# Kernel optimization log

Measured on AMD Instinct MI355X. Metric: run time of the kernel, lower is better.

## Reference

```python
import jax, jax.numpy as jnp
import numpy as np

SLOPE = 0.15  # LeakyReLU negative slope used throughout the module

def leaky(v):
    return jnp.where(v >= 0, v, SLOPE * v)

def _linear_params(key, fan_in, fan_out):
    kw, kb = jax.random.split(key)
    bound = 1.0 / np.sqrt(fan_in)
    W = jax.random.uniform(kw, (fan_in, fan_out), minval=-bound, maxval=bound, dtype=jnp.float32)
    b = jax.random.uniform(kb, (fan_out,), minval=-bound, maxval=bound, dtype=jnp.float32)
    return W, b

N_NODES = 50000
N_EDGES = 640000
IN_DIM = 128
EDGE_DIM = 64
HID = 128
LAT = 64

def setup_inputs() -> dict:
    key = jax.random.key(0)
    ks = jax.random.split(key, 12)
    x = jax.random.normal(ks[0], (N_NODES, IN_DIM), dtype=jnp.float32)
    edge_index = jax.random.randint(ks[1], (2, N_EDGES), 0, N_NODES, dtype=jnp.int32)
    edge_attr = jax.random.normal(ks[2], (N_EDGES, EDGE_DIM), dtype=jnp.float32)
    # conv1 params
    e1W1, e1b1 = _linear_params(ks[3], EDGE_DIM, HID)
    e1W2, e1b2 = _linear_params(ks[4], HID, HID)
    n1W, n1b = _linear_params(ks[5], IN_DIM + HID, HID)
    # conv2 params
    e2W1, e2b1 = _linear_params(ks[6], EDGE_DIM, HID)
    e2W2, e2b2 = _linear_params(ks[7], HID, HID)
    n2W, n2b = _linear_params(ks[8], HID + HID, HID)
    muW, mub = _linear_params(ks[9], HID, LAT)
    lvW, lvb = _linear_params(ks[10], HID, LAT)
    return {"x": x, "edge_index": edge_index, "edge_attr": edge_attr,
            "e1W1": e1W1, "e1b1": e1b1, "e1W2": e1W2, "e1b2": e1b2, "n1W": n1W, "n1b": n1b,
            "e2W1": e2W1, "e2b1": e2b1, "e2W2": e2W2, "e2b2": e2b2, "n2W": n2W, "n2b": n2b,
            "muW": muW, "mub": mub, "lvW": lvW, "lvb": lvb}

def edge_encoder(x, edge_index, edge_attr, eW1, eb1, eW2, eb2, nW, nb):
    # edge MLP: Linear -> LeakyReLU(0.15) -> Linear
    emb = leaky(edge_attr @ eW1 + eb1) @ eW2 + eb2           # [E, H]
    dst = edge_index[1]                                       # PyG x_i = x[target]
    z = jnp.concatenate([x[dst], emb], axis=1)                # [E, in+H]
    msg = z @ nW + nb                                         # [E, H]
    return jax.ops.segment_sum(msg, dst, num_segments=x.shape[0])  # aggr='add'

def reference(x, edge_index, edge_attr,
              e1W1, e1b1, e1W2, e1b2, n1W, n1b,
              e2W1, e2b1, e2W2, e2b2, n2W, n2b,
              muW, mub, lvW, lvb):
    # Dropout is identity in eval mode.
    h = leaky(edge_encoder(x, edge_index, edge_attr, e1W1, e1b1, e1W2, e1b2, n1W, n1b))
    h = leaky(edge_encoder(h, edge_index, edge_attr, e2W1, e2b1, e2W2, e2b2, n2W, n2b))
    mu = h @ muW + mub
    logvar = h @ lvW + lvb
    return (mu, logvar)
```

## Files before the change

kernel.cpp:

```cpp
#include <hip/hip_runtime.h>

typedef __bf16 bf16x4 __attribute__((ext_vector_type(4)));
typedef __bf16 bf16x8 __attribute__((ext_vector_type(8)));
typedef float  f32x4  __attribute__((ext_vector_type(4)));

constexpr int N_NODES = 50000;
constexpr int N_EDGES = 640000;
constexpr int NTILES  = 98;
constexpr int NB_EDGE = 2500;

__device__ __forceinline__ float leaky(float v) { return v >= 0.f ? v : 0.15f * v; }

__global__ void prep_kernel(
    const float* __restrict__ e1W1, const float* __restrict__ e1b1,
    const float* __restrict__ e1W2, const float* __restrict__ e1b2,
    const float* __restrict__ n1W,  const float* __restrict__ n1b,
    const float* __restrict__ e2W1, const float* __restrict__ e2b1,
    const float* __restrict__ e2W2, const float* __restrict__ e2b2,
    const float* __restrict__ n2W,  const float* __restrict__ n2b,
    const float* __restrict__ muW,  const float* __restrict__ mub,
    const float* __restrict__ lvW,  const float* __restrict__ lvb,
    __bf16* __restrict__ packE, __bf16* __restrict__ packN1,
    __bf16* __restrict__ packN2, __bf16* __restrict__ packH,
    float* __restrict__ ebias, float* __restrict__ c1, float* __restrict__ c2,
    float* __restrict__ hbias)
{
    int bid = blockIdx.x;
    int lane = threadIdx.x;
    int quad = lane >> 4, low = lane & 15;

    if (bid < 32) {
        int ct = bid >> 1, kt = bid & 1;
        for (int j = 0; j < 8; ++j) {
            int k = kt * 32 + quad * 8 + j;
            int n = ct * 16 + low;
            float v = (n < 128) ? e1W1[k * 128 + n] : e2W1[k * 128 + (n - 128)];
            packE[((ct * 2 + kt) * 64 + lane) * 8 + j] = (__bf16)v;
        }
    } else if (bid < 160) {
        bool is1 = bid < 96;
        int tile = bid - (is1 ? 32 : 96);
        const float* nW  = is1 ? n1W  : n2W;
        const float* eW2 = is1 ? e1W2 : e2W2;
        __bf16* dst = is1 ? packN1 : packN2;
        int ct = tile >> 3, kt = tile & 7;
        for (int j = 0; j < 8; ++j) {
            int k = kt * 32 + quad * 8 + j;
            int n = ct * 16 + low;
            float v;
            if (k < 128) {
                v = nW[k * 128 + n];
            } else {
                int i = k - 128;
                float acc = 0.f;
                for (int k2 = 0; k2 < 128; ++k2)
                    acc += eW2[i * 128 + k2] * nW[(128 + k2) * 128 + n];
                v = acc;
            }
            dst[((ct * 8 + kt) * 64 + lane) * 8 + j] = (__bf16)v;
        }
    } else if (bid < 192) {
        int tile = bid - 160;
        int ct = tile >> 2, kt = tile & 3;
        for (int j = 0; j < 8; ++j) {
            int k = kt * 32 + quad * 8 + j;
            int n = ct * 16 + low;
            float v = (n < 64) ? muW[k * 64 + n] : lvW[k * 64 + (n - 64)];
            packH[((ct * 4 + kt) * 64 + lane) * 8 + j] = (__bf16)v;
        }
    } else if (bid == 192 || bid == 193) {
        const float* nW  = (bid == 192) ? n1W  : n2W;
        const float* nb  = (bid == 192) ? n1b  : n2b;
        const float* eb2 = (bid == 192) ? e1b2 : e2b2;
        float* dst = (bid == 192) ? c1 : c2;
        for (int rep = 0; rep < 2; ++rep) {
            int j = lane + rep * 64;
            float acc = nb[j];
            for (int k = 0; k < 128; ++k)
                acc += eb2[k] * nW[(128 + k) * 128 + j];
            dst[j] = acc;
        }
    } else {
        for (int rep = 0; rep < 4; ++rep) {
            int j = lane + rep * 64;
            ebias[j] = (j < 128) ? e1b1[j] : e2b1[j - 128];
        }
        for (int rep = 0; rep < 2; ++rep) {
            int j = lane + rep * 64;
            hbias[j] = (j < 64) ? mub[j] : lvb[j - 64];
        }
    }
}

__global__ void hist_kernel(const int* __restrict__ dstp, int* __restrict__ deg) {
    int e = blockIdx.x * 256 + threadIdx.x;
    if (e < N_EDGES) atomicAdd(&deg[dstp[e]], 1);
}

__global__ void scan_a(const int* __restrict__ deg, int* __restrict__ offs,
                       int* __restrict__ tileSum) {
    __shared__ int s[512];
    int t = threadIdx.x, i = blockIdx.x * 512 + t;
    int v = (i < N_NODES) ? deg[i] : 0;
    s[t] = v; __syncthreads();
    for (int off = 1; off < 512; off <<= 1) {
        int x = (t >= off) ? s[t - off] : 0;
        __syncthreads();
        s[t] += x;
        __syncthreads();
    }
    if (i < N_NODES) offs[i] = s[t] - v;
    if (t == 511) tileSum[blockIdx.x] = s[511];
}

__global__ void scan_b(const int* __restrict__ tileSum, int* __restrict__ tileOff) {
    __shared__ int s[128];
    int t = threadIdx.x;
    int v = (t < NTILES) ? tileSum[t] : 0;
    s[t] = v; __syncthreads();
    for (int off = 1; off < 128; off <<= 1) {
        int x = (t >= off) ? s[t - off] : 0;
        __syncthreads();
        s[t] += x;
        __syncthreads();
    }
    if (t < NTILES) tileOff[t] = s[t] - v;
}

__global__ void scan_c(int* __restrict__ offs, const int* __restrict__ tileOff,
                       const int* __restrict__ deg, float* __restrict__ degf) {
    int i = blockIdx.x * 256 + threadIdx.x;
    if (i < N_NODES) {
        offs[i] += tileOff[i >> 9];
        degf[i] = (float)deg[i];
    }
}

__global__ void scatter_kernel(const int* __restrict__ dstp, const int* __restrict__ offs,
                               int* __restrict__ cursor, int* __restrict__ sorted,
                               int* __restrict__ sdst) {
    int e = blockIdx.x * 256 + threadIdx.x;
    if (e < N_EDGES) {
        int d = dstp[e];
        int p = offs[d] + atomicAdd(&cursor[d], 1);
        sorted[p] = e;
        sdst[p] = d;
    }
}

__global__ __launch_bounds__(256, 3) void edge_kernel(
    const float* __restrict__ edge_attr,
    const int* __restrict__ sorted, const int* __restrict__ sdst,
    const __bf16* __restrict__ packE,
    const float* __restrict__ ebias, float* __restrict__ S)
{
    __shared__ alignas(16) __bf16 As[64 * 72];
    __shared__ alignas(16) __bf16 Lball[4 * 64 * 72];
    __shared__ alignas(8) unsigned char runof_s[64];
    __shared__ int rundst_s[64];
    __shared__ int nruns_s;

    int tid = threadIdx.x;
    int w = tid >> 6, lane = tid & 63;
    int quad = lane >> 4, low = lane & 15;
    int r = tid >> 2, c0 = (tid & 3) * 16;

    bf16x8 bfragE[2][4];
    #pragma unroll
    for (int kt = 0; kt < 2; ++kt)
        #pragma unroll
        for (int ct = 0; ct < 4; ++ct)
            bfragE[kt][ct] = *reinterpret_cast<const bf16x8*>(
                packE + (((w * 4 + ct) * 2 + kt) * 64 + lane) * 8);
    float bias_c[4];
    #pragma unroll
    for (int ct = 0; ct < 4; ++ct) bias_c[ct] = ebias[w * 64 + ct * 16 + low];

    __bf16* Lb = &Lball[w * 4608];

    constexpr int STRIDE = NB_EDGE * 64;
    int e0 = blockIdx.x * 64;

    float4 f0, f1, f2, f3;
    int md_c, ei_n, md_n;
    {
        int ei = sorted[e0 + r];
        md_c = sdst[e0 + lane];
        const float4* ap = reinterpret_cast<const float4*>(edge_attr + (size_t)ei * 64 + c0);
        f0 = ap[0]; f1 = ap[1]; f2 = ap[2]; f3 = ap[3];
    }
    ei_n = sorted[e0 + STRIDE + r];
    md_n = sdst[e0 + STRIDE + lane];

    #pragma unroll 1
    for (int it = 0; it < 4; ++it) {
        {
            bf16x8 v0, v1;
            v0[0]=(__bf16)f0.x; v0[1]=(__bf16)f0.y; v0[2]=(__bf16)f0.z; v0[3]=(__bf16)f0.w;
            v0[4]=(__bf16)f1.x; v0[5]=(__bf16)f1.y; v0[6]=(__bf16)f1.z; v0[7]=(__bf16)f1.w;
            v1[0]=(__bf16)f2.x; v1[1]=(__bf16)f2.y; v1[2]=(__bf16)f2.z; v1[3]=(__bf16)f2.w;
            v1[4]=(__bf16)f3.x; v1[5]=(__bf16)f3.y; v1[6]=(__bf16)f3.z; v1[7]=(__bf16)f3.w;
            *reinterpret_cast<bf16x8*>(&As[r * 72 + c0])     = v0;
            *reinterpret_cast<bf16x8*>(&As[r * 72 + c0 + 8]) = v1;
        }

        if (w == 0) {
            rundst_s[lane] = md_c;
            int dp = __shfl_up(md_c, 1);
            bool flag = (lane > 0) && (md_c != dp);
            unsigned long long mask = __ballot(flag);
            int rid = __popcll(mask & ((1ull << lane) - 1ull)) + (flag ? 1 : 0);
            runof_s[lane] = (unsigned char)rid;
            if (flag || lane == 0) rundst_s[rid] = md_c;
            if (lane == 0) nruns_s = __popcll(mask) + 1;
        }
        __syncthreads();

        float4 g0{}, g1{}, g2{}, g3{};
        if (it < 3) {
            const float4* gp = reinterpret_cast<const float4*>(
                edge_attr + (size_t)ei_n * 64 + c0);
            g0 = gp[0]; g1 = gp[1]; g2 = gp[2]; g3 = gp[3];
        }
        int ei_nn = 0, md_nn = 0;
        if (it < 2) {
            int eo = e0 + (it + 2) * STRIDE;
            ei_nn = sorted[eo + r];
            md_nn = sdst[eo + lane];
        }

        f32x4 C1[4][4] = {};
        #pragma unroll
        for (int kt = 0; kt < 2; ++kt)
            #pragma unroll
            for (int rt = 0; rt < 4; ++rt) {
                bf16x8 a = *reinterpret_cast<const bf16x8*>(
                    &As[(rt * 16 + low) * 72 + kt * 32 + quad * 8]);
                #pragma unroll
                for (int ct = 0; ct < 4; ++ct)
                    C1[rt][ct] = __builtin_amdgcn_mfma_f32_16x16x32_bf16(
                        a, bfragE[kt][ct], C1[rt][ct], 0, 0, 0);
            }

        #pragma unroll
        for (int rt = 0; rt < 4; ++rt)
            #pragma unroll
            for (int ct = 0; ct < 4; ++ct) {
                bf16x4 v;
                #pragma unroll
                for (int rr = 0; rr < 4; ++rr)
                    v[rr] = (__bf16)leaky(C1[rt][ct][rr] + bias_c[ct]);
                *reinterpret_cast<bf16x4*>(
                    &Lb[(ct * 16 + low) * 72 + rt * 16 + quad * 4]) = v;
            }

        int nruns = nruns_s;
        for (int rt2 = 0; rt2 * 16 < nruns; ++rt2) {
            f32x4 C2[4] = {};
            #pragma unroll
            for (int kt = 0; kt < 2; ++kt) {
                uint2 rb = *reinterpret_cast<const uint2*>(&runof_s[kt * 32 + quad * 8]);
                unsigned target = (unsigned)(rt2 * 16 + low);
                bf16x8 a;
                #pragma unroll
                for (int j = 0; j < 8; ++j) {
                    unsigned byte = ((j < 4 ? (rb.x >> (8 * j)) : (rb.y >> (8 * (j - 4)))) & 0xFFu);
                    a[j] = (byte == target) ? (__bf16)1.0f : (__bf16)0.0f;
                }
                #pragma unroll
                for (int ct = 0; ct < 4; ++ct) {
                    bf16x8 b = *reinterpret_cast<const bf16x8*>(
                        &Lb[(ct * 16 + low) * 72 + kt * 32 + quad * 8]);
                    C2[ct] = __builtin_amdgcn_mfma_f32_16x16x32_bf16(a, b, C2[ct], 0, 0, 0);
                }
            }
            #pragma unroll
            for (int ct = 0; ct < 4; ++ct) {
                int col = w * 64 + ct * 16 + low;
                #pragma unroll
                for (int rr = 0; rr < 4; ++rr) {
                    int run = rt2 * 16 + quad * 4 + rr;
                    if (run < nruns) {
                        int node = rundst_s[run];
                        if ((unsigned)node < (unsigned)N_NODES)
                            unsafeAtomicAdd(&S[(size_t)node * 256 + col], C2[ct][rr]);
                    }
                }
            }
        }
        __syncthreads();

        f0 = g0; f1 = g1; f2 = g2; f3 = g3;
        md_c = md_n; ei_n = ei_nn; md_n = md_nn;
    }
}

template<int KT, int KT1, bool SCALE, bool ACT, bool SPLIT>
__global__ __launch_bounds__(256) void node_gemm(
    const float* __restrict__ A1, int lda1,
    const float* __restrict__ A2, int lda2,
    const float* __restrict__ degf,
    const __bf16* __restrict__ Bpack, const float* __restrict__ bias,
    float* __restrict__ out)
{
    int w = threadIdx.x >> 6, lane = threadIdx.x & 63;
    int quad = lane >> 4, low = lane & 15;
    int rb = blockIdx.x * 64 + w * 16;

    int arow = rb + low;
    if (arow >= N_NODES) arow = N_NODES - 1;
    float s = 1.f;
    if (SCALE) s = degf[arow];

    f32x4 C[8] = {};
    #pragma unroll
    for (int kt = 0; kt < KT; ++kt) {
        const float* base;
        if (kt < KT1) base = A1 + (size_t)arow * lda1 + kt * 32 + quad * 8;
        else          base = A2 + (size_t)arow * lda2 + (kt - KT1) * 32 + quad * 8;
        float4 p0 = *reinterpret_cast<const float4*>(base);
        float4 p1 = *reinterpret_cast<const float4*>(base + 4);
        float m = (SCALE && kt < KT1) ? s : 1.f;
        bf16x8 a;
        a[0] = (__bf16)(p0.x * m); a[1] = (__bf16)(p0.y * m);
        a[2] = (__bf16)(p0.z * m); a[3] = (__bf16)(p0.w * m);
        a[4] = (__bf16)(p1.x * m); a[5] = (__bf16)(p1.y * m);
        a[6] = (__bf16)(p1.z * m); a[7] = (__bf16)(p1.w * m);
        #pragma unroll
        for (int ct = 0; ct < 8; ++ct) {
            bf16x8 b = *reinterpret_cast<const bf16x8*>(Bpack + ((ct * KT + kt) * 64 + lane) * 8);
            C[ct] = __builtin_amdgcn_mfma_f32_16x16x32_bf16(a, b, C[ct], 0, 0, 0);
        }
    }

    #pragma unroll
    for (int ct = 0; ct < 8; ++ct) {
        int col = ct * 16 + low;
        #pragma unroll
        for (int rr = 0; rr < 4; ++rr) {
            int row = rb + quad * 4 + rr;
            if (row >= N_NODES) continue;
            float bb = bias[col];
            if (SCALE) bb *= degf[row];
            float v = C[ct][rr] + bb;
            if (ACT) v = leaky(v);
            if (SPLIT) {
                if (col < 64) out[(size_t)row * 64 + col] = v;
                else          out[(size_t)N_NODES * 64 + (size_t)row * 64 + (col - 64)] = v;
            } else {
                out[(size_t)row * 128 + col] = v;
            }
        }
    }
}

extern "C" void kernel_launch(void* const* d_in, const int* in_sizes, int n_in,
                              void* d_out, int out_size, void* d_ws, size_t ws_size,
                              hipStream_t stream)
{
    const float* x     = (const float*)d_in[0];
    const int*   eidx  = (const int*)  d_in[1];
    const float* eattr = (const float*)d_in[2];
    const float* e1W1 = (const float*)d_in[3];
    const float* e1b1 = (const float*)d_in[4];
    const float* e1W2 = (const float*)d_in[5];
    const float* e1b2 = (const float*)d_in[6];
    const float* n1W  = (const float*)d_in[7];
    const float* n1b  = (const float*)d_in[8];
    const float* e2W1 = (const float*)d_in[9];
    const float* e2b1 = (const float*)d_in[10];
    const float* e2W2 = (const float*)d_in[11];
    const float* e2b2 = (const float*)d_in[12];
    const float* n2W  = (const float*)d_in[13];
    const float* n2b  = (const float*)d_in[14];
    const float* muW  = (const float*)d_in[15];
    const float* mub  = (const float*)d_in[16];
    const float* lvW  = (const float*)d_in[17];
    const float* lvb  = (const float*)d_in[18];

    const int* dstp = eidx + N_EDGES;

    char* ws = (char*)d_ws;
    size_t off = 0;
    auto alloc = [&](size_t bytes) -> void* {
        void* p = ws + off;
        off = (off + bytes + 1023) & ~(size_t)1023;
        return p;
    };
    float* S       = (float*)alloc((size_t)N_NODES * 256 * 4);
    float* h       = (float*)alloc((size_t)N_NODES * 128 * 4);
    float* g       = (float*)alloc((size_t)N_NODES * 128 * 4);
    int*   deg     = (int*)  alloc((size_t)N_NODES * 4);
    int*   cursor  = (int*)  alloc((size_t)N_NODES * 4);
    int*   offs    = (int*)  alloc((size_t)N_NODES * 4);
    float* degf    = (float*)alloc((size_t)N_NODES * 4);
    int*   sorted  = (int*)  alloc((size_t)N_EDGES * 4);
    int*   tileSum = (int*)  alloc(NTILES * 4);
    int*   tileOff = (int*)  alloc(NTILES * 4);
    __bf16* packE  = (__bf16*)alloc(32 * 64 * 8 * 2);
    __bf16* packN1 = (__bf16*)alloc(64 * 64 * 8 * 2);
    __bf16* packN2 = (__bf16*)alloc(64 * 64 * 8 * 2);
    __bf16* packH  = (__bf16*)alloc(32 * 64 * 8 * 2);
    float* ebias   = (float*)alloc(256 * 4);
    float* c1      = (float*)alloc(128 * 4);
    float* c2      = (float*)alloc(128 * 4);
    float* hbias   = (float*)alloc(128 * 4);
    (void)ws_size; (void)in_sizes; (void)n_in; (void)out_size;

    int* sdst = (int*)g;

    hipMemsetAsync(S, 0, (size_t)N_NODES * 256 * 4, stream);
    hipMemsetAsync(deg, 0, 2 * (((size_t)N_NODES * 4 + 1023) & ~(size_t)1023), stream);

    prep_kernel<<<195, 64, 0, stream>>>(e1W1, e1b1, e1W2, e1b2, n1W, n1b,
                                        e2W1, e2b1, e2W2, e2b2, n2W, n2b,
                                        muW, mub, lvW, lvb,
                                        packE, packN1, packN2, packH,
                                        ebias, c1, c2, hbias);

    hist_kernel<<<N_EDGES / 256, 256, 0, stream>>>(dstp, deg);
    scan_a<<<NTILES, 512, 0, stream>>>(deg, offs, tileSum);
    scan_b<<<1, 128, 0, stream>>>(tileSum, tileOff);
    scan_c<<<(N_NODES + 255) / 256, 256, 0, stream>>>(offs, tileOff, deg, degf);
    scatter_kernel<<<N_EDGES / 256, 256, 0, stream>>>(dstp, offs, cursor, sorted, sdst);

    edge_kernel<<<NB_EDGE, 256, 0, stream>>>(eattr, sorted, sdst, packE, ebias, S);

    node_gemm<8, 4, true, true, false><<<(N_NODES + 63) / 64, 256, 0, stream>>>(
        x, 128, S, 256, degf, packN1, c1, h);
    node_gemm<8, 4, true, true, false><<<(N_NODES + 63) / 64, 256, 0, stream>>>(
        h, 128, S + 128, 256, degf, packN2, c2, g);
    node_gemm<4, 4, false, false, true><<<(N_NODES + 63) / 64, 256, 0, stream>>>(
        g, 128, g, 128, degf, packH, hbias, (float*)d_out);
}
```

Before: 490.4 us.

## Fuse three node GEMMs into one kernel and merge scan_c into neighbors

Replaces the three node_gemm launches with one node_fused kernel. It keeps each warp's 16-row intermediate activations in shared memory as bf16 and chains the conv1, conv2 and mu/logvar GEMMs, so the h and g intermediates never round-trip through global memory. scan_c is removed: degf is written in scan_a and the tile offset is added inside scatter. The edge kernel aliases As onto Lball, adding a __syncthreads, which lowers shared memory and lets the launch bound rise to 4 blocks per SM. The risks are extra register pressure in the fused kernel and the added barrier in the edge loop.

Result: slower. 538.1 us (+9.7%).

```diff
diff --git a/kernel.cpp b/kernel.cpp
--- a/kernel.cpp
+++ b/kernel.cpp
@@ -98,10 +98,11 @@
 }
 
 __global__ void scan_a(const int* __restrict__ deg, int* __restrict__ offs,
-                       int* __restrict__ tileSum) {
+                       int* __restrict__ tileSum, float* __restrict__ degf) {
     __shared__ int s[512];
     int t = threadIdx.x, i = blockIdx.x * 512 + t;
     int v = (i < N_NODES) ? deg[i] : 0;
+    if (i < N_NODES) degf[i] = (float)v;
     s[t] = v; __syncthreads();
     for (int off = 1; off < 512; off <<= 1) {
         int x = (t >= off) ? s[t - off] : 0;
@@ -127,34 +128,25 @@
     if (t < NTILES) tileOff[t] = s[t] - v;
 }
 
-__global__ void scan_c(int* __restrict__ offs, const int* __restrict__ tileOff,
-                       const int* __restrict__ deg, float* __restrict__ degf) {
-    int i = blockIdx.x * 256 + threadIdx.x;
-    if (i < N_NODES) {
-        offs[i] += tileOff[i >> 9];
-        degf[i] = (float)deg[i];
-    }
-}
-
 __global__ void scatter_kernel(const int* __restrict__ dstp, const int* __restrict__ offs,
+                               const int* __restrict__ tileOff,
                                int* __restrict__ cursor, int* __restrict__ sorted,
                                int* __restrict__ sdst) {
     int e = blockIdx.x * 256 + threadIdx.x;
     if (e < N_EDGES) {
         int d = dstp[e];
-        int p = offs[d] + atomicAdd(&cursor[d], 1);
+        int p = offs[d] + tileOff[d >> 9] + atomicAdd(&cursor[d], 1);
         sorted[p] = e;
         sdst[p] = d;
     }
 }
 
-__global__ __launch_bounds__(256, 3) void edge_kernel(
+__global__ __launch_bounds__(256, 4) void edge_kernel(
     const float* __restrict__ edge_attr,
     const int* __restrict__ sorted, const int* __restrict__ sdst,
     const __bf16* __restrict__ packE,
     const float* __restrict__ ebias, float* __restrict__ S)
 {
-    __shared__ alignas(16) __bf16 As[64 * 72];
     __shared__ alignas(16) __bf16 Lball[4 * 64 * 72];
     __shared__ alignas(8) unsigned char runof_s[64];
     __shared__ int rundst_s[64];
@@ -176,6 +168,7 @@
     #pragma unroll
     for (int ct = 0; ct < 4; ++ct) bias_c[ct] = ebias[w * 64 + ct * 16 + low];
 
+    __bf16* As = Lball;
     __bf16* Lb = &Lball[w * 4608];
 
     constexpr int STRIDE = NB_EDGE * 64;
@@ -241,6 +234,7 @@
                     C1[rt][ct] = __builtin_amdgcn_mfma_f32_16x16x32_bf16(
                         a, bfragE[kt][ct], C1[rt][ct], 0, 0, 0);
             }
+        __syncthreads();
 
         #pragma unroll
         for (int rt = 0; rt < 4; ++rt)
@@ -259,12 +253,12 @@
             f32x4 C2[4] = {};
             #pragma unroll
             for (int kt = 0; kt < 2; ++kt) {
-                uint2 rb = *reinterpret_cast<const uint2*>(&runof_s[kt * 32 + quad * 8]);
+                uint2 rb2 = *reinterpret_cast<const uint2*>(&runof_s[kt * 32 + quad * 8]);
                 unsigned target = (unsigned)(rt2 * 16 + low);
                 bf16x8 a;
                 #pragma unroll
                 for (int j = 0; j < 8; ++j) {
-                    unsigned byte = ((j < 4 ? (rb.x >> (8 * j)) : (rb.y >> (8 * (j - 4)))) & 0xFFu);
+                    unsigned byte = ((j < 4 ? (rb2.x >> (8 * j)) : (rb2.y >> (8 * (j - 4)))) & 0xFFu);
                     a[j] = (byte == target) ? (__bf16)1.0f : (__bf16)0.0f;
                 }
                 #pragma unroll
@@ -295,61 +289,115 @@
     }
 }
 
-template<int KT, int KT1, bool SCALE, bool ACT, bool SPLIT>
-__global__ __launch_bounds__(256) void node_gemm(
-    const float* __restrict__ A1, int lda1,
-    const float* __restrict__ A2, int lda2,
+__global__ __launch_bounds__(256) void node_fused(
+    const float* __restrict__ x, const float* __restrict__ S,
     const float* __restrict__ degf,
-    const __bf16* __restrict__ Bpack, const float* __restrict__ bias,
+    const __bf16* __restrict__ packN1, const __bf16* __restrict__ packN2,
+    const __bf16* __restrict__ packH,
+    const float* __restrict__ c1, const float* __restrict__ c2,
+    const float* __restrict__ hbias,
     float* __restrict__ out)
 {
+    constexpr int HS = 152;
+    __shared__ __bf16 Hs[4][16 * HS];
     int w = threadIdx.x >> 6, lane = threadIdx.x & 63;
     int quad = lane >> 4, low = lane & 15;
     int rb = blockIdx.x * 64 + w * 16;
 
     int arow = rb + low;
     if (arow >= N_NODES) arow = N_NODES - 1;
-    float s = 1.f;
-    if (SCALE) s = degf[arow];
+    float ds = degf[arow];
+    const float* xrow = x + (size_t)arow * 128;
+    const float* Srow = S + (size_t)arow * 256;
+
+    float deg4[4];
+    #pragma unroll
+    for (int rr = 0; rr < 4; ++rr) {
+        int row = rb + quad * 4 + rr;
+        deg4[rr] = degf[row < N_NODES ? row : N_NODES - 1];
+    }
+
+    __bf16* Hw = Hs[w];
 
     f32x4 C[8] = {};
     #pragma unroll
-    for (int kt = 0; kt < KT; ++kt) {
-        const float* base;
-        if (kt < KT1) base = A1 + (size_t)arow * lda1 + kt * 32 + quad * 8;
-        else          base = A2 + (size_t)arow * lda2 + (kt - KT1) * 32 + quad * 8;
+    for (int kt = 0; kt < 8; ++kt) {
+        const float* base = (kt < 4) ? (xrow + kt * 32 + quad * 8)
+                                     : (Srow + (kt - 4) * 32 + quad * 8);
         float4 p0 = *reinterpret_cast<const float4*>(base);
         float4 p1 = *reinterpret_cast<const float4*>(base + 4);
-        float m = (SCALE && kt < KT1) ? s : 1.f;
+        float m = (kt < 4) ? ds : 1.f;
         bf16x8 a;
-        a[0] = (__bf16)(p0.x * m); a[1] = (__bf16)(p0.y * m);
-        a[2] = (__bf16)(p0.z * m); a[3] = (__bf16)(p0.w * m);
-        a[4] = (__bf16)(p1.x * m); a[5] = (__bf16)(p1.y * m);
-        a[6] = (__bf16)(p1.z * m); a[7] = (__bf16)(p1.w * m);
+        a[0]=(__bf16)(p0.x*m); a[1]=(__bf16)(p0.y*m); a[2]=(__bf16)(p0.z*m); a[3]=(__bf16)(p0.w*m);
+        a[4]=(__bf16)(p1.x*m); a[5]=(__bf16)(p1.y*m); a[6]=(__bf16)(p1.z*m); a[7]=(__bf16)(p1.w*m);
         #pragma unroll
         for (int ct = 0; ct < 8; ++ct) {
-            bf16x8 b = *reinterpret_cast<const bf16x8*>(Bpack + ((ct * KT + kt) * 64 + lane) * 8);
+            bf16x8 b = *reinterpret_cast<const bf16x8*>(packN1 + ((ct * 8 + kt) * 64 + lane) * 8);
             C[ct] = __builtin_amdgcn_mfma_f32_16x16x32_bf16(a, b, C[ct], 0, 0, 0);
         }
     }
-
     #pragma unroll
     for (int ct = 0; ct < 8; ++ct) {
         int col = ct * 16 + low;
+        float cb = c1[col];
+        #pragma unroll
+        for (int rr = 0; rr < 4; ++rr) {
+            float v = leaky(C[ct][rr] + deg4[rr] * cb);
+            Hw[(quad * 4 + rr) * HS + col] = (__bf16)(v * deg4[rr]);
+        }
+    }
+
+    f32x4 C2[8] = {};
+    #pragma unroll
+    for (int kt = 0; kt < 8; ++kt) {
+        bf16x8 a;
+        if (kt < 4) {
+            a = *reinterpret_cast<const bf16x8*>(&Hw[low * HS + kt * 32 + quad * 8]);
+        } else {
+            const float* base = Srow + 128 + (kt - 4) * 32 + quad * 8;
+            float4 p0 = *reinterpret_cast<const float4*>(base);
+            float4 p1 = *reinterpret_cast<const float4*>(base + 4);
+            a[0]=(__bf16)p0.x; a[1]=(__bf16)p0.y; a[2]=(__bf16)p0.z; a[3]=(__bf16)p0.w;
+            a[4]=(__bf16)p1.x; a[5]=(__bf16)p1.y; a[6]=(__bf16)p1.z; a[7]=(__bf16)p1.w;
+        }
+        #pragma unroll
+        for (int ct = 0; ct < 8; ++ct) {
+            bf16x8 b = *reinterpret_cast<const bf16x8*>(packN2 + ((ct * 8 + kt) * 64 + lane) * 8);
+            C2[ct] = __builtin_amdgcn_mfma_f32_16x16x32_bf16(a, b, C2[ct], 0, 0, 0);
+        }
+    }
+    #pragma unroll
+    for (int ct = 0; ct < 8; ++ct) {
+        int col = ct * 16 + low;
+        float cb = c2[col];
+        #pragma unroll
+        for (int rr = 0; rr < 4; ++rr) {
+            float v = leaky(C2[ct][rr] + deg4[rr] * cb);
+            Hw[(quad * 4 + rr) * HS + col] = (__bf16)v;
+        }
+    }
+
+    f32x4 C3[8] = {};
+    #pragma unroll
+    for (int kt = 0; kt < 4; ++kt) {
+        bf16x8 a = *reinterpret_cast<const bf16x8*>(&Hw[low * HS + kt * 32 + quad * 8]);
+        #pragma unroll
+        for (int ct = 0; ct < 8; ++ct) {
+            bf16x8 b = *reinterpret_cast<const bf16x8*>(packH + ((ct * 4 + kt) * 64 + lane) * 8);
+            C3[ct] = __builtin_amdgcn_mfma_f32_16x16x32_bf16(a, b, C3[ct], 0, 0, 0);
+        }
+    }
+    #pragma unroll
+    for (int ct = 0; ct < 8; ++ct) {
+        int col = ct * 16 + low;
+        float hb = hbias[col];
         #pragma unroll
         for (int rr = 0; rr < 4; ++rr) {
             int row = rb + quad * 4 + rr;
             if (row >= N_NODES) continue;
-            float bb = bias[col];
-            if (SCALE) bb *= degf[row];
-            float v = C[ct][rr] + bb;
-            if (ACT) v = leaky(v);
-            if (SPLIT) {
-                if (col < 64) out[(size_t)row * 64 + col] = v;
-                else          out[(size_t)N_NODES * 64 + (size_t)row * 64 + (col - 64)] = v;
-            } else {
-                out[(size_t)row * 128 + col] = v;
-            }
+            float v = C3[ct][rr] + hb;
+            if (col < 64) out[(size_t)row * 64 + col] = v;
+            else          out[(size_t)N_NODES * 64 + (size_t)row * 64 + (col - 64)] = v;
         }
     }
 }
@@ -405,7 +453,7 @@
     float* c1      = (float*)alloc(128 * 4);
     float* c2      = (float*)alloc(128 * 4);
     float* hbias   = (float*)alloc(128 * 4);
-    (void)ws_size; (void)in_sizes; (void)n_in; (void)out_size;
+    (void)ws_size; (void)in_sizes; (void)n_in; (void)out_size; (void)h;
 
     int* sdst = (int*)g;
 
@@ -419,17 +467,12 @@
                                         ebias, c1, c2, hbias);
 
     hist_kernel<<<N_EDGES / 256, 256, 0, stream>>>(dstp, deg);
-    scan_a<<<NTILES, 512, 0, stream>>>(deg, offs, tileSum);
+    scan_a<<<NTILES, 512, 0, stream>>>(deg, offs, tileSum, degf);
     scan_b<<<1, 128, 0, stream>>>(tileSum, tileOff);
-    scan_c<<<(N_NODES + 255) / 256, 256, 0, stream>>>(offs, tileOff, deg, degf);
-    scatter_kernel<<<N_EDGES / 256, 256, 0, stream>>>(dstp, offs, cursor, sorted, sdst);
+    scatter_kernel<<<N_EDGES / 256, 256, 0, stream>>>(dstp, offs, tileOff, cursor, sorted, sdst);
 
     edge_kernel<<<NB_EDGE, 256, 0, stream>>>(eattr, sorted, sdst, packE, ebias, S);
 
-    node_gemm<8, 4, true, true, false><<<(N_NODES + 63) / 64, 256, 0, stream>>>(
-        x, 128, S, 256, degf, packN1, c1, h);
-    node_gemm<8, 4, true, true, false><<<(N_NODES + 63) / 64, 256, 0, stream>>>(
-        h, 128, S + 128, 256, degf, packN2, c2, g);
-    node_gemm<4, 4, false, false, true><<<(N_NODES + 63) / 64, 256, 0, stream>>>(
-        g, 128, g, 128, degf, packH, hbias, (float*)d_out);
-}
+    node_fused<<<(N_NODES + 63) / 64, 256, 0, stream>>>(
+        x, S, degf, packN1, packN2, packH, c1, c2, hbias, (float*)d_out);
+}
```
